# Optimization experiments

Measured on AMD Instinct MI355X. Metric: run time of the kernel, lower is better.

The kernel has to match this reference:

```python
import jax, jax.numpy as jnp
import numpy as np

LN_EPS = 1e-5
NEG_INF = -1e30


def setup_inputs() -> dict:
    key = jax.random.key(0)
    k_adj, k_feat, k_mask, k_w = jax.random.split(key, 4)
    B, N, H, R, L = 8, 400, 768, 46, 2
    adj = jax.random.uniform(k_adj, (B, N, N, R), dtype=jnp.float32)
    feature = jax.random.normal(k_feat, (B, N, H), dtype=jnp.float32)
    dmask = (jax.random.uniform(k_mask, (B, 1, N)) > 0.1).astype(jnp.float32)
    # per-layer, per-relation Linear(H, H, bias=False) weights, applied as x @ W
    W = jax.random.normal(k_w, (L, R, H, H), dtype=jnp.float32) / np.sqrt(H)
    return {"adj": adj, "feature": feature, "dmask": dmask, "W": W}


def reference(adj, feature, dmask, W):
    # adj: [B,N,N,R] -> [B,R,N,N]; dmask: [B,1,N] masks key/column axis
    B, N, _, R = adj.shape
    a = jnp.transpose(adj, (0, 3, 1, 2))           # [B,R,N,N]
    m = dmask[:, None, :, :]                        # [B,1,1,N]
    logits = a * m + (1.0 - m) * NEG_INF
    att = jax.nn.softmax(logits, axis=-1)           # [B,R,N,N] (layer-invariant)

    x = feature
    num_layers = W.shape[0]
    for layer in range(num_layers):
        # grouped per-relation linear: h[b,r,n,k] = feature[b,n,h] @ W[layer,r,h,k]
        h = jnp.einsum('bnh,rhk->brnk', x, W[layer])
        h = jax.nn.relu(jnp.einsum('brnm,brmk->brnk', att, h))
        addition = h.sum(axis=1)                    # sum over relations -> [B,N,H]
        z = jax.nn.relu(addition) / R
        # LayerNorm without affine params
        mu = jnp.mean(z, axis=-1, keepdims=True)
        var = jnp.var(z, axis=-1, keepdims=True)
        x = (z - mu) / jnp.sqrt(var + LN_EPS)
        # dropout is identity in eval mode
    return x
```

## Files before the change

### kernel.cpp

```cpp
#include <hip/hip_runtime.h>
#include <stdint.h>

#define BS 8
#define NN 400
#define HH 768
#define RR 46
#define MPAD 416
#define MFLAT2 3328
#define LDW2 3328
#define PADM 402

typedef _Float16 half8 __attribute__((ext_vector_type(8)));
typedef _Float16 half4v __attribute__((ext_vector_type(4)));
typedef float floatx4 __attribute__((ext_vector_type(4)));

__device__ __forceinline__ void async16(const void* g, void* l) {
  __builtin_amdgcn_global_load_lds((const __attribute__((address_space(1))) uint32_t*)g,
                                   (__attribute__((address_space(3))) uint32_t*)l, 16, 0, 0);
}

__device__ __forceinline__ int xcd_work(int flat, int nwg) {
  int q = nwg >> 3, rem = nwg & 7;
  int xcd = flat & 7, slot = flat >> 3;
  return (xcd < rem ? xcd * (q + 1) : rem * (q + 1) + (xcd - rem) * q) + slot;
}

__device__ __forceinline__ void vm_wait(int ahead) {
  if (ahead >= 2) asm volatile("s_waitcnt vmcnt(8)" ::: "memory");
  else if (ahead == 1) asm volatile("s_waitcnt vmcnt(4)" ::: "memory");
  else asm volatile("s_waitcnt vmcnt(0)" ::: "memory");
}
#define BAR_TOP() { __builtin_amdgcn_s_barrier(); __builtin_amdgcn_sched_barrier(0); }
#define BAR_BOT() { asm volatile("s_waitcnt lgkmcnt(0)" ::: "memory"); \
                    __builtin_amdgcn_s_barrier(); __builtin_amdgcn_sched_barrier(0); }

__device__ __forceinline__ void stage_tile(const _Float16* __restrict__ g, int ld, int rowbase,
                                           int maxrow, int kbase, _Float16* lds, int t) {
  int w = t >> 6, lane = t & 63;
#pragma unroll
  for (int j = 0; j < 2; ++j) {
    int chunk = w * 2 + j;
    int eo = chunk * 512 + lane * 8;
    int row = eo >> 5;
    int col = eo & 31;
    int grow = rowbase + row;
    grow = grow > maxrow ? maxrow : grow;
    async16(g + (size_t)grow * ld + kbase + col, lds + chunk * 512);
  }
}

__device__ __forceinline__ void mma_tiles(const _Float16* As, const _Float16* Bs, int lane,
                                          int wr, int wc, floatx4 acc[4][4]) {
  int arow = wr + (lane & 15);
  int brow = wc + (lane & 15);
  int kcol = (lane >> 4) * 8;
  half8 a[4], b[4];
#pragma unroll
  for (int i = 0; i < 4; ++i) a[i] = *(const half8*)&As[(arow + i * 16) * 32 + kcol];
#pragma unroll
  for (int i = 0; i < 4; ++i) b[i] = *(const half8*)&Bs[(brow + i * 16) * 32 + kcol];
#pragma unroll
  for (int i = 0; i < 4; ++i)
#pragma unroll
    for (int j = 0; j < 4; ++j)
      acc[i][j] = __builtin_amdgcn_mfma_f32_16x16x32_f16(a[i], b[j], acc[i][j], 0, 0, 0);
}

__global__ __launch_bounds__(256) void conv_w(const float* __restrict__ W, _Float16* __restrict__ Wt) {
  __shared__ float tl[32][33];
  int t = threadIdx.x;
  int lr = blockIdx.y;
  int tr = blockIdx.x / 24, tc = blockIdx.x % 24;
  const float* src = W + (size_t)lr * HH * HH;
  _Float16* dst = Wt + (size_t)lr * HH * HH;
  int rl = t >> 5, cl = t & 31;
#pragma unroll
  for (int j = 0; j < 4; ++j)
    tl[rl + 8 * j][cl] = src[(size_t)(tr * 32 + rl + 8 * j) * HH + tc * 32 + cl];
  __syncthreads();
#pragma unroll
  for (int j = 0; j < 4; ++j)
    dst[(size_t)(tc * 32 + rl + 8 * j) * HH + tr * 32 + cl] = (_Float16)tl[cl][rl + 8 * j];
}

__global__ void conv_x(const float* __restrict__ f, _Float16* __restrict__ x16) {
  int i4 = blockIdx.x * 256 + threadIdx.x;
  int row = i4 / 192;
  int c4 = i4 - row * 192;
  int b = row / 416;
  int m = row - b * 416;
  half4v h = {};
  if (m < NN) {
    float4 v = *(const float4*)(f + ((size_t)(b * NN + m) * HH) + c4 * 4);
    h[0] = (_Float16)v.x; h[1] = (_Float16)v.y; h[2] = (_Float16)v.z; h[3] = (_Float16)v.w;
  }
  *(half4v*)&x16[(size_t)row * HH + c4 * 4] = h;
}

__global__ __launch_bounds__(512) void att_softmax(const float* __restrict__ adj,
                                                   const float* __restrict__ dmask,
                                                   _Float16* __restrict__ att) {
  __shared__ _Float16 sE[RR * PADM];
  __shared__ float sM[NN];
  int t = threadIdx.x;
  int n = blockIdx.x, b = blockIdx.y;
  const float* arow = adj + ((size_t)b * NN + n) * NN * RR;
  for (int i = t; i < NN; i += 512) sM[i] = dmask[b * NN + i];
  __syncthreads();
  for (int e0 = t * 4; e0 < NN * RR; e0 += 2048) {
    float4 v = *(const float4*)(arow + e0);
    float vv[4] = {v.x, v.y, v.z, v.w};
#pragma unroll
    for (int j = 0; j < 4; ++j) {
      int e = e0 + j;
      int m = e / RR;
      int r = e - m * RR;
      float val = sM[m] > 0.5f ? __expf(vv[j]) : 0.0f;
      sE[r * PADM + m] = (_Float16)val;
    }
  }
  __syncthreads();
  int lane = t & 63, wid = t >> 6;
  for (int r = wid; r < RR; r += 8) {
    const _Float16* row = &sE[r * PADM];
    float s = 0.f;
    for (int m = lane; m < NN; m += 64) s += (float)row[m];
#pragma unroll
    for (int o = 32; o; o >>= 1) s += __shfl_xor(s, o);
    float inv = 1.0f / s;
    _Float16* orow = att + (((size_t)b * RR + r) * NN + n) * MPAD;
    for (int m2 = lane * 2; m2 < MPAD; m2 += 128) {
      _Float16 lo = (_Float16)0.f, hi = (_Float16)0.f;
      if (m2 < NN) lo = (_Float16)((float)row[m2] * inv);
      if (m2 + 1 < NN) hi = (_Float16)((float)row[m2 + 1] * inv);
      union { _Float16 h[2]; uint32_t u; } pk;
      pk.h[0] = lo; pk.h[1] = hi;
      *(uint32_t*)&orow[m2] = pk.u;
    }
  }
}

__global__ __launch_bounds__(256) void gemm_xw(const _Float16* __restrict__ x16,
                                               const _Float16* __restrict__ Wt,
                                               _Float16* __restrict__ h1T, int layer, int r0, int rbase) {
  __shared__ __align__(16) char smraw[49152];
  int t = threadIdx.x;
  int work = xcd_work(blockIdx.x, gridDim.x);
  int r_i = work / 156;
  int rem = work - r_i * 156;
  int r = r0 + r_i;
  int mtile = rem / 6, ntile = rem % 6;
  const _Float16* A = x16;
  const _Float16* Bp = Wt + ((size_t)layer * RR + r) * HH * HH;
  int lane = t & 63, w = t >> 6;
  int wr = (w >> 1) * 64, wc = (w & 1) * 64;
  floatx4 acc[4][4] = {};
  stage_tile(A, HH, mtile * 128, MFLAT2 - 1, 0, (_Float16*)smraw, t);
  stage_tile(Bp, HH, ntile * 128, HH - 1, 0, (_Float16*)(smraw + 8192), t);
  stage_tile(A, HH, mtile * 128, MFLAT2 - 1, 32, (_Float16*)(smraw + 16384), t);
  stage_tile(Bp, HH, ntile * 128, HH - 1, 32, (_Float16*)(smraw + 24576), t);
  int cur = 0, stb = 2;
  for (int ks = 0; ks < 24; ++ks) {
    if (ks + 2 < 24) {
      char* nb = smraw + stb * 16384;
      stage_tile(A, HH, mtile * 128, MFLAT2 - 1, (ks + 2) * 32, (_Float16*)nb, t);
      stage_tile(Bp, HH, ntile * 128, HH - 1, (ks + 2) * 32, (_Float16*)(nb + 8192), t);
      stb = stb == 2 ? 0 : stb + 1;
    }
    vm_wait(ks + 2 < 24 ? 2 : (ks + 1 < 24 ? 1 : 0));
    BAR_TOP();
    char* cb = smraw + cur * 16384;
    mma_tiles((const _Float16*)cb, (const _Float16*)(cb + 8192), lane, wr, wc, acc);
    BAR_BOT();
    cur = cur == 2 ? 0 : cur + 1;
  }
  _Float16* outl = (_Float16*)smraw;
#pragma unroll
  for (int i = 0; i < 4; ++i) {
#pragma unroll
    for (int j = 0; j < 4; ++j) {
      int rl = wr + i * 16 + (lane >> 4) * 4;
      int cl = wc + j * 16 + (lane & 15);
      half4v v = {(_Float16)acc[i][j][0], (_Float16)acc[i][j][1],
                  (_Float16)acc[i][j][2], (_Float16)acc[i][j][3]};
      *(half4v*)&outl[cl * 136 + rl] = v;
    }
  }
  __syncthreads();
  _Float16* outp = h1T + (size_t)(r - rbase) * HH * LDW2;
#pragma unroll
  for (int pass = 0; pass < 8; ++pass) {
    int c = pass * 16 + (t >> 4);
    int ml = (t & 15) * 8;
    int gm = mtile * 128 + ml;
    int gn = ntile * 128 + c;
    half8 v = *(const half8*)&outl[c * 136 + ml];
    *(half8*)&outp[(size_t)gn * LDW2 + gm] = v;
  }
}

__global__ __launch_bounds__(256) void gemm_att(const _Float16* __restrict__ att,
                                                const _Float16* __restrict__ h1T,
                                                float* __restrict__ partials, size_t psz,
                                                int rs, int rcount, int rbase, int accflag,
                                                int ngroups) {
  __shared__ __align__(16) char smraw[49152];
  int t = threadIdx.x;
  int work = xcd_work(blockIdx.x, gridDim.x);
  int ntile = work % 6;
  int tmp = work / 6;
  int mtile = tmp & 3; tmp >>= 2;
  int g = tmp % ngroups;
  int b = tmp / ngroups;
  int rbeg = rs + (g * rcount) / ngroups;
  int rend = rs + ((g + 1) * rcount) / ngroups;
  int nr = rend - rbeg;
  float* part = partials + (size_t)g * psz;
  int lane = t & 63, w = t >> 6;
  int wr = (w >> 1) * 64, wc = (w & 1) * 64;
  floatx4 acc[4][4] = {}, sum[4][4] = {};
  const _Float16* A0 = att + ((size_t)b * RR + rbeg) * NN * MPAD;
  const _Float16* B0 = h1T + (size_t)(rbeg - rbase) * HH * LDW2 + b * MPAD;
  int total = nr * 13;
  stage_tile(A0, MPAD, mtile * 128, NN - 1, 0, (_Float16*)smraw, t);
  stage_tile(B0, LDW2, ntile * 128, HH - 1, 0, (_Float16*)(smraw + 8192), t);
  stage_tile(A0, MPAD, mtile * 128, NN - 1, 32, (_Float16*)(smraw + 16384), t);
  stage_tile(B0, LDW2, ntile * 128, HH - 1, 32, (_Float16*)(smraw + 24576), t);
  const _Float16* nsA = A0;
  const _Float16* nsB = B0;
  int nsk = 2, cks = 0, cur = 0, stb = 2;
  if (total == 2) { nsk = 0; nsA += (size_t)NN * MPAD; nsB += (size_t)HH * LDW2; }
  for (int s = 0; s < total; ++s) {
    if (s + 2 < total) {
      char* nb = smraw + stb * 16384;
      stage_tile(nsA, MPAD, mtile * 128, NN - 1, nsk * 32, (_Float16*)nb, t);
      stage_tile(nsB, LDW2, ntile * 128, HH - 1, nsk * 32, (_Float16*)(nb + 8192), t);
      stb = stb == 2 ? 0 : stb + 1;
      if (++nsk == 13) { nsk = 0; nsA += (size_t)NN * MPAD; nsB += (size_t)HH * LDW2; }
    }
    vm_wait(s + 2 < total ? 2 : (s + 1 < total ? 1 : 0));
    BAR_TOP();
    char* cb = smraw + cur * 16384;
    mma_tiles((const _Float16*)cb, (const _Float16*)(cb + 8192), lane, wr, wc, acc);
    if (cks == 12) {
#pragma unroll
      for (int i = 0; i < 4; ++i)
#pragma unroll
        for (int j = 0; j < 4; ++j) {
#pragma unroll
          for (int q2 = 0; q2 < 4; ++q2) sum[i][j][q2] += fmaxf(acc[i][j][q2], 0.0f);
          acc[i][j] = (floatx4){0.f, 0.f, 0.f, 0.f};
        }
    }
    BAR_BOT();
    cur = cur == 2 ? 0 : cur + 1;
    cks = cks == 12 ? 0 : cks + 1;
  }
#pragma unroll
  for (int i = 0; i < 4; ++i) {
    int rl = wr + i * 16 + (lane >> 4) * 4;
    int grow = mtile * 128 + rl;
#pragma unroll
    for (int j = 0; j < 4; ++j) {
      int gcol = ntile * 128 + wc + j * 16 + (lane & 15);
#pragma unroll
      for (int q2 = 0; q2 < 4; ++q2) {
        if (grow + q2 < NN) {
          size_t idx = ((size_t)b * NN + grow + q2) * HH + gcol;
          float v = sum[i][j][q2];
          if (accflag) v += part[idx];
          part[idx] = v;
        }
      }
    }
  }
}

__global__ __launch_bounds__(256) void lnorm(const float* __restrict__ partials, size_t psz, int np,
                                             _Float16* __restrict__ x16, float* __restrict__ out) {
  int row = blockIdx.x;
  int t = threadIdx.x;
  int b = row / NN;
  int xrow = row + b * 16;
  float v[3];
  float s = 0.f, s2 = 0.f;
#pragma unroll
  for (int j = 0; j < 3; ++j) {
    float a = 0.f;
    for (int gidx = 0; gidx < np; ++gidx) a += partials[(size_t)gidx * psz + (size_t)row * HH + t + j * 256];
    v[j] = fmaxf(a, 0.f) * (1.0f / RR);
    s += v[j];
    s2 += v[j] * v[j];
  }
#pragma unroll
  for (int o = 32; o; o >>= 1) {
    s += __shfl_xor(s, o);
    s2 += __shfl_xor(s2, o);
  }
  __shared__ float rs_[4], rs2_[4];
  int lane = t & 63, wid = t >> 6;
  if (!lane) { rs_[wid] = s; rs2_[wid] = s2; }
  __syncthreads();
  s = rs_[0] + rs_[1] + rs_[2] + rs_[3];
  s2 = rs2_[0] + rs2_[1] + rs2_[2] + rs2_[3];
  float mu = s * (1.0f / HH);
  float var = s2 * (1.0f / HH) - mu * mu;
  float rstd = rsqrtf(var + 1e-5f);
#pragma unroll
  for (int j = 0; j < 3; ++j) {
    float o = (v[j] - mu) * rstd;
    out[(size_t)row * HH + t + j * 256] = o;
    x16[(size_t)xrow * HH + t + j * 256] = (_Float16)o;
  }
}

extern "C" void kernel_launch(void* const* d_in, const int* in_sizes, int n_in,
                              void* d_out, int out_size, void* d_ws, size_t ws_size,
                              hipStream_t stream) {
  const float* adj = (const float*)d_in[0];
  const float* feature = (const float*)d_in[1];
  const float* dmask = (const float*)d_in[2];
  const float* W = (const float*)d_in[3];
  float* out = (float*)d_out;

  uintptr_t base = (uintptr_t)d_ws;
  uintptr_t p = base;
  auto alloc = [&](size_t bytes) -> void* {
    uintptr_t q = (p + 255) & ~(uintptr_t)255;
    p = q + bytes;
    return (void*)q;
  };
  _Float16* att = (_Float16*)alloc((size_t)BS * RR * NN * MPAD * 2);
  _Float16* Wt = (_Float16*)alloc((size_t)2 * RR * HH * HH * 2);
  _Float16* x16 = (_Float16*)alloc((size_t)MFLAT2 * HH * 2);
  size_t psz = (size_t)(BS * NN) * HH;
  float* partials = (float*)alloc(4 * psz * 4);
  size_t used = p - base;
  size_t perR = (size_t)HH * LDW2 * 2;
  size_t avail = ws_size > used ? ws_size - used : 0;
  int RCmax = (int)(avail / perR);
  if (RCmax > RR) RCmax = RR;
  if (RCmax < 1) RCmax = 1;
  _Float16* h1T = (_Float16*)alloc((size_t)RCmax * perR);

  conv_w<<<dim3(576, 2 * RR), 256, 0, stream>>>(W, Wt);
  conv_x<<<MFLAT2 * HH / 4 / 256, 256, 0, stream>>>(feature, x16);
  att_softmax<<<dim3(NN, BS), 512, 0, stream>>>(adj, dmask, att);

  for (int layer = 0; layer < 2; ++layer) {
    if (RCmax >= RR) {
      gemm_xw<<<156 * RR, 256, 0, stream>>>(x16, Wt, h1T, layer, 0, 0);
      gemm_att<<<24 * 4 * BS, 256, 0, stream>>>(att, h1T, partials, psz, 0, RR, 0, 0, 4);
      lnorm<<<BS * NN, 256, 0, stream>>>(partials, psz, 4, x16, out);
    } else {
      for (int r0 = 0; r0 < RR; r0 += RCmax) {
        int rc = RR - r0 < RCmax ? RR - r0 : RCmax;
        gemm_xw<<<156 * rc, 256, 0, stream>>>(x16, Wt, h1T, layer, r0, r0);
        gemm_att<<<24 * 1 * BS, 256, 0, stream>>>(att, h1T, partials, psz, r0, rc, r0, r0 > 0, 1);
      }
      lnorm<<<BS * NN, 256, 0, stream>>>(partials, psz, 1, x16, out);
    }
  }
}
```

Baseline: 1.127 ms.

## Deepen gemm_att pipeline to 4 buffers with single barrier and more relation groups

The attention GEMM moves from 3-stage to 4-stage LDS buffering, keeping three tiles in flight, and uses one barrier per k-step instead of two. Staging addresses are precomputed per thread and advanced incrementally, and MFMA sections run at raised wave priority. The host grows the relation split from 4 to up to 8 groups when workspace allows, giving more workgroups at the cost of more partial buffers for lnorm to sum. The larger 64KB LDS footprint may reduce occupancy.

```diff
diff --git a/kernel.cpp b/kernel.cpp
--- a/kernel.cpp
+++ b/kernel.cpp
@@ -26,13 +26,15 @@
 }
 
 __device__ __forceinline__ void vm_wait(int ahead) {
-  if (ahead >= 2) asm volatile("s_waitcnt vmcnt(8)" ::: "memory");
+  if (ahead >= 3) asm volatile("s_waitcnt vmcnt(12)" ::: "memory");
+  else if (ahead == 2) asm volatile("s_waitcnt vmcnt(8)" ::: "memory");
   else if (ahead == 1) asm volatile("s_waitcnt vmcnt(4)" ::: "memory");
   else asm volatile("s_waitcnt vmcnt(0)" ::: "memory");
 }
 #define BAR_TOP() { __builtin_amdgcn_s_barrier(); __builtin_amdgcn_sched_barrier(0); }
 #define BAR_BOT() { asm volatile("s_waitcnt lgkmcnt(0)" ::: "memory"); \
                     __builtin_amdgcn_s_barrier(); __builtin_amdgcn_sched_barrier(0); }
+#define BAR_ONE() { asm volatile("s_barrier" ::: "memory"); __builtin_amdgcn_sched_barrier(0); }
 
 __device__ __forceinline__ void stage_tile(const _Float16* __restrict__ g, int ld, int rowbase,
                                            int maxrow, int kbase, _Float16* lds, int t) {
@@ -204,7 +206,7 @@
                                                 float* __restrict__ partials, size_t psz,
                                                 int rs, int rcount, int rbase, int accflag,
                                                 int ngroups) {
-  __shared__ __align__(16) char smraw[49152];
+  __shared__ __align__(16) char smraw[65536];
   int t = threadIdx.x;
   int work = xcd_work(blockIdx.x, gridDim.x);
   int ntile = work % 6;
@@ -222,26 +224,43 @@
   const _Float16* A0 = att + ((size_t)b * RR + rbeg) * NN * MPAD;
   const _Float16* B0 = h1T + (size_t)(rbeg - rbase) * HH * LDW2 + b * MPAD;
   int total = nr * 13;
-  stage_tile(A0, MPAD, mtile * 128, NN - 1, 0, (_Float16*)smraw, t);
-  stage_tile(B0, LDW2, ntile * 128, HH - 1, 0, (_Float16*)(smraw + 8192), t);
-  stage_tile(A0, MPAD, mtile * 128, NN - 1, 32, (_Float16*)(smraw + 16384), t);
-  stage_tile(B0, LDW2, ntile * 128, HH - 1, 32, (_Float16*)(smraw + 24576), t);
-  const _Float16* nsA = A0;
-  const _Float16* nsB = B0;
-  int nsk = 2, cks = 0, cur = 0, stb = 2;
-  if (total == 2) { nsk = 0; nsA += (size_t)NN * MPAD; nsB += (size_t)HH * LDW2; }
+
+  int srow = lane >> 2, scol = (lane & 3) * 8;
+  int c0 = w * 2;
+  int ga0 = mtile * 128 + c0 * 16 + srow;       ga0 = ga0 > NN - 1 ? NN - 1 : ga0;
+  int ga1 = mtile * 128 + (c0 + 1) * 16 + srow; ga1 = ga1 > NN - 1 ? NN - 1 : ga1;
+  int gb0 = ntile * 128 + c0 * 16 + srow;
+  int gb1 = ntile * 128 + (c0 + 1) * 16 + srow;
+  const _Float16* pa0 = A0 + (size_t)ga0 * MPAD + scol;
+  const _Float16* pa1 = A0 + (size_t)ga1 * MPAD + scol;
+  const _Float16* pb0 = B0 + (size_t)gb0 * LDW2 + scol;
+  const _Float16* pb1 = B0 + (size_t)gb1 * LDW2 + scol;
+  int nsk = 0;
+
+  auto issue = [&](int buf) {
+    _Float16* lA = (_Float16*)(smraw + buf * 16384) + c0 * 512;
+    _Float16* lB = (_Float16*)(smraw + buf * 16384 + 8192) + c0 * 512;
+    async16(pa0, lA); async16(pa1, lA + 512);
+    async16(pb0, lB); async16(pb1, lB + 512);
+    if (++nsk == 13) {
+      nsk = 0;
+      pa0 += (size_t)NN * MPAD - 384; pa1 += (size_t)NN * MPAD - 384;
+      pb0 += (size_t)HH * LDW2 - 384; pb1 += (size_t)HH * LDW2 - 384;
+    } else {
+      pa0 += 32; pa1 += 32; pb0 += 32; pb1 += 32;
+    }
+  };
+
+  issue(0); issue(1); issue(2);
+  vm_wait(2);
+  BAR_ONE();
+  int cks = 0;
   for (int s = 0; s < total; ++s) {
-    if (s + 2 < total) {
-      char* nb = smraw + stb * 16384;
-      stage_tile(nsA, MPAD, mtile * 128, NN - 1, nsk * 32, (_Float16*)nb, t);
-      stage_tile(nsB, LDW2, ntile * 128, HH - 1, nsk * 32, (_Float16*)(nb + 8192), t);
-      stb = stb == 2 ? 0 : stb + 1;
-      if (++nsk == 13) { nsk = 0; nsA += (size_t)NN * MPAD; nsB += (size_t)HH * LDW2; }
-    }
-    vm_wait(s + 2 < total ? 2 : (s + 1 < total ? 1 : 0));
-    BAR_TOP();
-    char* cb = smraw + cur * 16384;
+    if (s + 3 < total) issue((s + 3) & 3);
+    char* cb = smraw + (s & 3) * 16384;
+    __builtin_amdgcn_s_setprio(1);
     mma_tiles((const _Float16*)cb, (const _Float16*)(cb + 8192), lane, wr, wc, acc);
+    __builtin_amdgcn_s_setprio(0);
     if (cks == 12) {
 #pragma unroll
       for (int i = 0; i < 4; ++i)
@@ -251,10 +270,13 @@
           for (int q2 = 0; q2 < 4; ++q2) sum[i][j][q2] += fmaxf(acc[i][j][q2], 0.0f);
           acc[i][j] = (floatx4){0.f, 0.f, 0.f, 0.f};
         }
-    }
-    BAR_BOT();
-    cur = cur == 2 ? 0 : cur + 1;
-    cks = cks == 12 ? 0 : cks + 1;
+      cks = 0;
+    } else ++cks;
+    if (s + 1 < total) {
+      int ahead = total - s - 2;
+      vm_wait(ahead > 2 ? 2 : ahead);
+      BAR_ONE();
+    }
   }
 #pragma unroll
   for (int i = 0; i < 4; ++i) {
@@ -334,29 +356,38 @@
   _Float16* Wt = (_Float16*)alloc((size_t)2 * RR * HH * HH * 2);
   _Float16* x16 = (_Float16*)alloc((size_t)MFLAT2 * HH * 2);
   size_t psz = (size_t)(BS * NN) * HH;
-  float* partials = (float*)alloc(4 * psz * 4);
+  size_t pszB = psz * 4;
   size_t used = p - base;
+  size_t rem = ws_size > used ? ws_size - used : 0;
   size_t perR = (size_t)HH * LDW2 * 2;
-  size_t avail = ws_size > used ? ws_size - used : 0;
-  int RCmax = (int)(avail / perR);
-  if (RCmax > RR) RCmax = RR;
-  if (RCmax < 1) RCmax = 1;
-  _Float16* h1T = (_Float16*)alloc((size_t)RCmax * perR);
+  size_t h1full = (size_t)RR * perR;
 
   conv_w<<<dim3(576, 2 * RR), 256, 0, stream>>>(W, Wt);
   conv_x<<<MFLAT2 * HH / 4 / 256, 256, 0, stream>>>(feature, x16);
   att_softmax<<<dim3(NN, BS), 512, 0, stream>>>(adj, dmask, att);
 
-  for (int layer = 0; layer < 2; ++layer) {
-    if (RCmax >= RR) {
+  if (rem >= h1full + 4 * pszB + 512) {
+    _Float16* h1T = (_Float16*)alloc(h1full);
+    int ngroups = (int)(((ws_size - (p - base)) - 256) / pszB);
+    if (ngroups > 8) ngroups = 8;
+    float* partials = (float*)alloc((size_t)ngroups * pszB);
+    for (int layer = 0; layer < 2; ++layer) {
       gemm_xw<<<156 * RR, 256, 0, stream>>>(x16, Wt, h1T, layer, 0, 0);
-      gemm_att<<<24 * 4 * BS, 256, 0, stream>>>(att, h1T, partials, psz, 0, RR, 0, 0, 4);
-      lnorm<<<BS * NN, 256, 0, stream>>>(partials, psz, 4, x16, out);
-    } else {
+      gemm_att<<<6 * 4 * ngroups * BS, 256, 0, stream>>>(att, h1T, partials, psz, 0, RR, 0, 0, ngroups);
+      lnorm<<<BS * NN, 256, 0, stream>>>(partials, psz, ngroups, x16, out);
+    }
+  } else {
+    float* partials = (float*)alloc(pszB);
+    size_t rem2 = ws_size > (p - base) ? ws_size - (p - base) : 0;
+    int RCmax = (int)(rem2 / perR);
+    if (RCmax > RR) RCmax = RR;
+    if (RCmax < 1) RCmax = 1;
+    _Float16* h1T = (_Float16*)alloc((size_t)RCmax * perR);
+    for (int layer = 0; layer < 2; ++layer) {
       for (int r0 = 0; r0 < RR; r0 += RCmax) {
         int rc = RR - r0 < RCmax ? RR - r0 : RCmax;
         gemm_xw<<<156 * rc, 256, 0, stream>>>(x16, Wt, h1T, layer, r0, r0);
-        gemm_att<<<24 * 1 * BS, 256, 0, stream>>>(att, h1T, partials, psz, r0, rc, r0, r0 > 0, 1);
+        gemm_att<<<6 * 4 * 1 * BS, 256, 0, stream>>>(att, h1T, partials, psz, r0, rc, r0, r0 > 0, 1);
       }
       lnorm<<<BS * NN, 256, 0, stream>>>(partials, psz, 1, x16, out);
     }
```

Measured after the change: 1.141 ms. No clear change (+1.2%).
